# Kernel optimization log

Hardware: AMD Instinct MI355X
Metric: run time of the kernel (lower is better)

The kernel has to match this reference:

```python
import jax, jax.numpy as jnp
import numpy as np

B, T, S, E, H, V, OOV = 16, 32, 400, 128, 512, 32000, 50


def setup_inputs() -> dict:
    key = jax.random.key(0)
    ks = jax.random.split(key, 24)
    sc = 0.05
    inp = {
        'input_embeddings': jax.random.normal(ks[0], (B, T, E), jnp.float32),
        'h0': jax.random.normal(ks[1], (B, H), jnp.float32) * sc,
        'c0': jax.random.normal(ks[2], (B, H), jnp.float32) * sc,
        'encoder_outputs': jax.random.normal(ks[3], (B, S, H), jnp.float32),
        'encoder_masks': jnp.ones((B, S), jnp.float32),
        'extra_zeros': jnp.zeros((B, OOV), jnp.float32),
        'extended_source_idx': jax.random.randint(ks[4], (B, S), 0, V + OOV),
        # LSTM cell params (torch gate order i,f,g,o)
        'W_ih': jax.random.normal(ks[5], (4 * H, E), jnp.float32) * sc,
        'W_hh': jax.random.normal(ks[6], (4 * H, H), jnp.float32) * sc,
        'b_ih': jax.random.normal(ks[7], (4 * H,), jnp.float32) * sc,
        'b_hh': jax.random.normal(ks[8], (4 * H,), jnp.float32) * sc,
        # vocab projection
        'W_vocab': jax.random.normal(ks[9], (V, H), jnp.float32) * sc,
        'b_vocab': jax.random.normal(ks[10], (V,), jnp.float32) * sc,
        # attention: coverage_linear (H,1), energy_linear (H, 2H), v (H)
        'W_cov': jax.random.normal(ks[11], (H, 1), jnp.float32) * sc,
        'W_energy': jax.random.normal(ks[12], (H, 2 * H), jnp.float32) * sc,
        'b_energy': jax.random.normal(ks[13], (H,), jnp.float32) * sc,
        'v_attn': jax.random.uniform(ks[14], (H,), jnp.float32),
        # x_context: (E, E+H)
        'W_xctx': jax.random.normal(ks[15], (E, E + H), jnp.float32) * sc,
        'b_xctx': jax.random.normal(ks[16], (E,), jnp.float32) * sc,
        # attention_dense: (H, 2H)
        'W_ad': jax.random.normal(ks[17], (H, 2 * H), jnp.float32) * sc,
        'b_ad': jax.random.normal(ks[18], (H,), jnp.float32) * sc,
        # p_gen: (1, H + H + E)
        'W_pgen': jax.random.normal(ks[19], (1, 2 * H + E), jnp.float32) * sc,
        'b_pgen': jax.random.normal(ks[20], (1,), jnp.float32) * sc,
    }
    return inp


def _forward(input_embeddings, h0, c0, encoder_outputs, encoder_masks, extra_zeros,
             W_ih, W_hh, b_ih, b_hh, W_vocab, b_vocab, W_cov, W_energy, b_energy,
             v_attn, W_xctx, b_xctx, W_ad, b_ad, W_pgen, b_pgen, extended_source_idx):
    Bc, Sc_, Hc = encoder_outputs.shape
    oov = extra_zeros.shape[1]
    # split energy linear into decoder-part and encoder-part (cat order: [dec, enc])
    W_d, W_e = W_energy[:, :Hc], W_energy[:, Hc:]
    # encoder projection computed ONCE (same math as per-step recompute)
    enc_proj = jnp.einsum('bsh,kh->bsk', encoder_outputs, W_e) + b_energy  # [B,S,H]
    w_cov = W_cov[:, 0]  # [H]
    rows = jnp.arange(Bc)[:, None]

    def step(carry, emb_t):
        h, c, ctx, cov = carry  # [B,H],[B,H],[B,H],[B,S]
        x = jnp.concatenate([emb_t, ctx], -1) @ W_xctx.T + b_xctx  # [B,E]
        gates = x @ W_ih.T + b_ih + h @ W_hh.T + b_hh
        i_g, f_g, g_g, o_g = jnp.split(gates, 4, axis=-1)
        c = jax.nn.sigmoid(f_g) * c + jax.nn.sigmoid(i_g) * jnp.tanh(g_g)
        h = jax.nn.sigmoid(o_g) * jnp.tanh(c)
        # additive attention with coverage
        dec_proj = h @ W_d.T  # [B,H]
        cov_feat = cov[:, :, None] * w_cov[None, None, :]  # [B,S,H]
        energy = jnp.tanh(dec_proj[:, None, :] + enc_proj + cov_feat)
        score = jnp.einsum('bsh,h->bs', energy, v_attn)
        probs = jax.nn.softmax(score, axis=-1) * encoder_masks
        probs = probs / (probs.sum(-1, keepdims=True) + 1e-12)
        ctx = jnp.einsum('bs,bsh->bh', probs, encoder_outputs)
        cov = cov + probs
        # vocab distribution
        hh = jnp.concatenate([h, ctx], -1) @ W_ad.T + b_ad
        vocab_dist = jax.nn.softmax(hh @ W_vocab.T + b_vocab, axis=-1)  # [B,V]
        # pointer-generator mix
        p_gen = jax.nn.sigmoid(jnp.concatenate([ctx, h, x], -1) @ W_pgen.T + b_pgen)  # [B,1]
        attn_ = (1.0 - p_gen) * probs  # [B,S]
        ext = jnp.concatenate([vocab_dist * p_gen, extra_zeros], axis=1)  # [B,V+oov]
        final = ext.at[rows, extended_source_idx].add(attn_)
        return (h, c, ctx, cov), (final, probs, cov)

    init = (h0, c0, jnp.zeros_like(h0), jnp.zeros((Bc, Sc_), h0.dtype))
    (_, _, _, _), (finals, attns, covs) = jax.lax.scan(
        step, init, jnp.swapaxes(input_embeddings, 0, 1))
    return jnp.swapaxes(finals, 0, 1)  # [B,T,V+oov]


def reference(input_embeddings, h0, c0, encoder_outputs, encoder_masks, extra_zeros,
              extended_source_idx, W_ih, W_hh, b_ih, b_hh, W_vocab, b_vocab,
              W_cov, W_energy, b_energy, v_attn, W_xctx, b_xctx, W_ad, b_ad,
              W_pgen, b_pgen):
    return _forward(input_embeddings, h0, c0, encoder_outputs, encoder_masks,
                    extra_zeros, W_ih, W_hh, b_ih, b_hh, W_vocab, b_vocab,
                    W_cov, W_energy, b_energy, v_attn, W_xctx, b_xctx,
                    W_ad, b_ad, W_pgen, b_pgen, extended_source_idx)
```

## Files before the change

kernel.cpp:

```cpp
#include <hip/hip_runtime.h>
#include <hip/hip_bf16.h>
#include <cstddef>

namespace {

constexpr int B = 16, T = 32, S = 400, E = 128, H = 512, V = 32000, OOV = 50, VEXT = V + OOV;

typedef __attribute__((ext_vector_type(8))) short short8v;
typedef __attribute__((ext_vector_type(4))) float f32x4;

__device__ __forceinline__ float fsig(float x){ return 1.0f/(1.0f+__expf(-x)); }
__device__ __forceinline__ float ftanh(float x){
  float ax = fabsf(x);
  float t = __expf(-2.0f*ax);
  float r = (1.0f - t)/(1.0f + t);
  return copysignf(r, x);
}
__device__ __forceinline__ unsigned short f2bf(float f){
  unsigned int u = __float_as_uint(f);
  unsigned int r = (u + 0x7FFFu + ((u >> 16) & 1u)) >> 16;
  return (unsigned short)r;
}
__device__ __forceinline__ float bf2f(unsigned short u){
  return __uint_as_float(((unsigned)u) << 16);
}

__global__ __launch_bounds__(256) void k_init(const float* __restrict__ enc,
    const float* __restrict__ h0, const float* __restrict__ c0,
    unsigned short* __restrict__ enc_bf, float* __restrict__ harr,
    float* __restrict__ cbuf, float* __restrict__ cov, float* __restrict__ vsum){
  const int stride = gridDim.x*256;
  for (int i = blockIdx.x*256 + threadIdx.x; i < B*S*H; i += stride){
    enc_bf[i] = f2bf(enc[i]);
    if (i < B*H){ harr[i] = h0[i]; cbuf[i] = c0[i]; }
    if (i < B*S) cov[i] = 0.0f;
    if (i < T*B) vsum[i] = 0.0f;
  }
}

__global__ __launch_bounds__(128) void k_x0(const float* __restrict__ emb,
    const float* __restrict__ W_xctx, const float* __restrict__ b_xctx,
    float* __restrict__ x0){
  const int b = blockIdx.x, tid = threadIdx.x;
  __shared__ float se[E];
  se[tid] = emb[(size_t)(b*T)*E + tid];
  __syncthreads();
  const float* w = W_xctx + (size_t)tid*(E+H);
  float acc = b_xctx[tid];
  #pragma unroll 8
  for (int k=0;k<E;k+=4){
    float4 wv = *reinterpret_cast<const float4*>(w+k);
    acc += se[k]*wv.x + se[k+1]*wv.y + se[k+2]*wv.z + se[k+3]*wv.w;
  }
  x0[b*E + tid] = acc;
}

__global__ __launch_bounds__(256) void k_trw2(const float* __restrict__ W_energy,
    float* __restrict__ Wt, float* __restrict__ WdT){
  __shared__ float tile[32][33];
  const int z = blockIdx.z;
  float* out = z ? WdT : Wt;
  const int off = z ? 0 : H;
  const int j0 = blockIdx.x*32, k0 = blockIdx.y*32;
  const int tx = threadIdx.x & 31, ty = threadIdx.x >> 5;
  #pragma unroll
  for (int r=0;r<4;++r)
    tile[ty+8*r][tx] = W_energy[(size_t)(k0+ty+8*r)*(2*H) + off + j0 + tx];
  __syncthreads();
  #pragma unroll
  for (int r=0;r<4;++r)
    out[(size_t)(j0+ty+8*r)*H + k0 + tx] = tile[tx][ty+8*r];
}

__global__ __launch_bounds__(512) void k_encproj(const float* __restrict__ enc,
                          const float* __restrict__ Wt,
                          const float* __restrict__ b_energy,
                          unsigned short* __restrict__ enc_proj){
  const int r0 = blockIdx.x*16, k = threadIdx.x;
  const float* eb = enc + (size_t)r0*H;
  float acc[16];
  #pragma unroll
  for (int r=0;r<16;++r) acc[r]=0.0f;
  for (int j=0;j<H;j+=4){
    const float w0 = Wt[(size_t) j   *H + k];
    const float w1 = Wt[(size_t)(j+1)*H + k];
    const float w2 = Wt[(size_t)(j+2)*H + k];
    const float w3 = Wt[(size_t)(j+3)*H + k];
    #pragma unroll
    for (int r=0;r<16;++r){
      acc[r] += eb[(size_t)r*H + j]*w0 + eb[(size_t)r*H + j+1]*w1
              + eb[(size_t)r*H + j+2]*w2 + eb[(size_t)r*H + j+3]*w3;
    }
  }
  const float be = b_energy[k];
  #pragma unroll
  for (int r=0;r<16;++r) enc_proj[(size_t)(r0+r)*H + k] = f2bf(acc[r] + be);
}

__global__ __launch_bounds__(256) void k_gates2(
    const float* __restrict__ x, const float* __restrict__ hold,
    const float* __restrict__ W_ih, const float* __restrict__ W_hh,
    float* __restrict__ gpart){
  const int blk = blockIdx.x, tid = threadIdx.x;
  const int gbh = blk >> 2, kh = blk & 3;
  const int gb = gbh >> 1, bh = gbh & 1, b0 = bh*8;
  __shared__ float xh[8][640];
  __shared__ float sg[4][64][9];
  for (int b=0;b<8;++b)
    for (int k=tid;k<640;k+=256)
      xh[b][k] = (k<E) ? x[(b0+b)*E + k] : hold[(b0+b)*H + (k-E)];
  __syncthreads();
  const int w = tid >> 6, l = tid & 63, g = l >> 4, jj = l & 15;
  const int row = g*H + gb*16 + jj;
  float acc[8];
  #pragma unroll
  for (int b=0;b<8;++b) acc[b]=0.0f;
  const int ks = kh*160 + w*40, ke = ks + 40;
  const int k1 = (ke < 128) ? ke : 128;
  if (ks < 128){
    const float* wr = W_ih + (size_t)row*E;
    for (int k=ks; k<k1; k+=4){
      const float4 wv = *reinterpret_cast<const float4*>(wr + k);
      #pragma unroll
      for (int b=0;b<8;++b){
        const float4 xv = *reinterpret_cast<const float4*>(&xh[b][k]);
        acc[b] += xv.x*wv.x + xv.y*wv.y + xv.z*wv.z + xv.w*wv.w;
      }
    }
  }
  const int k2 = (ks > 128) ? ks : 128;
  if (k2 < ke){
    const float* wr = W_hh + (size_t)row*H - 128;
    for (int k=k2; k<ke; k+=4){
      const float4 wv = *reinterpret_cast<const float4*>(wr + k);
      #pragma unroll
      for (int b=0;b<8;++b){
        const float4 xv = *reinterpret_cast<const float4*>(&xh[b][k]);
        acc[b] += xv.x*wv.x + xv.y*wv.y + xv.z*wv.z + xv.w*wv.w;
      }
    }
  }
  #pragma unroll
  for (int b=0;b<8;++b) sg[w][l][b] = acc[b];
  __syncthreads();
  for (int i=tid; i<512; i+=256){
    const int l2 = i & 63, b = i >> 6;
    const int g2 = l2 >> 4, j2 = l2 & 15;
    const int row2 = g2*H + gb*16 + j2;
    gpart[((size_t)kh*B + (b0+b))*(4*H) + row2] =
        sg[0][l2][b]+sg[1][l2][b]+sg[2][l2][b]+sg[3][l2][b];
  }
}

__global__ __launch_bounds__(256) void k_dec2(const float* __restrict__ gpart,
    const float* __restrict__ cold, const float* __restrict__ b_ih,
    const float* __restrict__ b_hh, const float* __restrict__ WdT,
    float* __restrict__ cnew, float* __restrict__ hnew, float* __restrict__ dec){
  const int blk = blockIdx.x, tid = threadIdx.x;
  const int jc = blk >> 3, bp = blk & 7, b0 = bp*2;
  __shared__ float sh[2][H];
  __shared__ float r[4][64][2];
  for (int i=tid; i<2*H; i+=256){
    const int bl = i >> 9, j = i & 511;
    const int b = b0 + bl;
    float gs[4];
    #pragma unroll
    for (int g=0; g<4; ++g){
      const int row = g*H + j;
      float v = b_ih[row] + b_hh[row];
      #pragma unroll
      for (int kh=0; kh<4; ++kh) v += gpart[((size_t)kh*B + b)*(4*H) + row];
      gs[g] = v;
    }
    const float ig = fsig(gs[0]);
    const float fg = fsig(gs[1]);
    const float gg = ftanh(gs[2]);
    const float og = fsig(gs[3]);
    const float cn = fg*cold[b*H + j] + ig*gg;
    const float hn = og*ftanh(cn);
    cnew[b*H + j] = cn;
    hnew[b*H + j] = hn;
    sh[bl][j] = hn;
  }
  __syncthreads();
  const int w = tid >> 6, lane = tid & 63;
  const int j = jc*64 + lane;
  float a0=0.0f, a1=0.0f;
  for (int k=w*128; k<w*128+128; ++k){
    const float wv = WdT[(size_t)k*H + j];
    a0 += sh[0][k]*wv;
    a1 += sh[1][k]*wv;
  }
  r[w][lane][0]=a0; r[w][lane][1]=a1;
  __syncthreads();
  if (tid < 128){
    const int jl = tid & 63, bb = tid >> 6;
    dec[(b0+bb)*H + jc*64 + jl] = r[0][jl][bb]+r[1][jl][bb]+r[2][jl][bb]+r[3][jl][bb];
  }
}

__global__ __launch_bounds__(256) void k_score(const float* __restrict__ dec_proj,
    const unsigned short* __restrict__ encp, const float* __restrict__ W_cov,
    const float* __restrict__ v_attn, const float* __restrict__ cov,
    float* __restrict__ score, float* __restrict__ xnext){
  const int b = blockIdx.y;
  if (blockIdx.x==0 && threadIdx.x < E) xnext[b*E + threadIdx.x] = 0.0f;
  const int wave = threadIdx.x >> 6, lane = threadIdx.x & 63;
  const int s = blockIdx.x*4 + wave;
  const float cv = cov[b*S + s];
  const int k0 = lane*8;
  const short8v ev = *reinterpret_cast<const short8v*>(encp + (size_t)(b*S + s)*H + k0);
  const float* dp = dec_proj + b*H;
  float acc = 0.0f;
  #pragma unroll
  for (int u=0;u<8;++u){
    const int k = k0+u;
    acc += ftanh(dp[k] + bf2f((unsigned short)ev[u]) + cv*W_cov[k]) * v_attn[k];
  }
  #pragma unroll
  for (int off=32; off>0; off>>=1) acc += __shfl_down(acc, off);
  if (lane==0) score[b*S + s] = acc;
}

__global__ __launch_bounds__(256) void k_ctx(const float* __restrict__ score,
    const float* __restrict__ masks, const unsigned short* __restrict__ enc_bf,
    const float* __restrict__ emb, int tnext,
    const float* __restrict__ W_xctx, const float* __restrict__ b_xctx,
    float* __restrict__ cov, float* __restrict__ probs_t,
    float* __restrict__ ctx_t, float* __restrict__ xnext){
  const int b = blockIdx.x, hc = blockIdx.y, tid = threadIdx.x;
  __shared__ float red[256], sp[512], sctx[64], se[E];
  if (tid < E) se[tid] = emb[(size_t)(b*T + tnext)*E + tid];
  const float sc0 = (tid < S)      ? score[b*S + tid]       : -1e30f;
  const float sc1 = (tid+256 < S)  ? score[b*S + tid + 256] : -1e30f;
  red[tid] = fmaxf(sc0, sc1);
  __syncthreads();
  for (int off=128; off>0; off>>=1){ if (tid<off) red[tid]=fmaxf(red[tid],red[tid+off]); __syncthreads(); }
  const float mx = red[0];
  __syncthreads();
  const float e0 = (tid < S)     ? __expf(sc0 - mx) : 0.0f;
  const float e1 = (tid+256 < S) ? __expf(sc1 - mx) : 0.0f;
  red[tid] = e0 + e1;
  __syncthreads();
  for (int off=128; off>0; off>>=1){ if (tid<off) red[tid]+=red[tid+off]; __syncthreads(); }
  const float den = red[0];
  __syncthreads();
  const float p0 = (tid < S)     ? (e0/den)*masks[b*S+tid]     : 0.0f;
  const float p1 = (tid+256 < S) ? (e1/den)*masks[b*S+tid+256] : 0.0f;
  red[tid] = p0 + p1;
  __syncthreads();
  for (int off=128; off>0; off>>=1){ if (tid<off) red[tid]+=red[tid+off]; __syncthreads(); }
  const float inv = 1.0f/(red[0] + 1e-12f);
  __syncthreads();
  const float pr0 = p0*inv, pr1 = p1*inv;
  sp[tid] = pr0; sp[tid+256] = pr1;
  if (hc==0){
    if (tid < S){ probs_t[b*S+tid] = pr0; cov[b*S+tid] += pr0; }
    if (tid+256 < S){ probs_t[b*S+tid+256] = pr1; cov[b*S+tid+256] += pr1; }
  }
  __syncthreads();
  {
    const int c = tid & 63, sg_ = tid >> 6;
    const unsigned short* eb = enc_bf + (size_t)b*S*H + hc*64 + c;
    float a = 0.0f;
    for (int s=sg_; s<S; s+=4) a += sp[s]*bf2f(eb[(size_t)s*H]);
    red[tid] = a;
    __syncthreads();
    if (tid < 64){
      const float cval = red[tid]+red[tid+64]+red[tid+128]+red[tid+192];
      sctx[tid] = cval;
      ctx_t[b*H + hc*64 + tid] = cval;
    }
  }
  __syncthreads();
  if (tid < E){
    const float* wr = W_xctx + (size_t)tid*(E+H);
    float acc = 0.0f;
    #pragma unroll
    for (int k=0;k<64;k+=4){
      const float4 wc = *reinterpret_cast<const float4*>(wr + E + hc*64 + k);
      acc += sctx[k]*wc.x + sctx[k+1]*wc.y + sctx[k+2]*wc.z + sctx[k+3]*wc.w;
    }
    #pragma unroll
    for (int k=0;k<16;k+=4){
      const float4 we = *reinterpret_cast<const float4*>(wr + hc*16 + k);
      const float* eb2 = se + hc*16 + k;
      acc += eb2[0]*we.x + eb2[1]*we.y + eb2[2]*we.z + eb2[3]*we.w;
    }
    if (hc==0) acc += b_xctx[tid];
    atomicAdd(&xnext[b*E + tid], acc);
  }
}

__global__ __launch_bounds__(512) void k_hhgemm(const float* __restrict__ harr,
    const float* __restrict__ ctx_all, const float* __restrict__ W_ad,
    const float* __restrict__ b_ad, float* __restrict__ hh_all){
  __shared__ unsigned short ldsA[256][72];
  __shared__ unsigned short ldsB[128][72];
  const int tid = threadIdx.x, lane = tid & 63, w = tid >> 6;
  const int wm = w >> 1, wn = w & 1;
  const int m0 = (int)blockIdx.y * 256;
  const int n0 = (int)blockIdx.x * 128;
  const int nl = lane & 15, kg = lane >> 4;
  f32x4 acc[4][4];
  #pragma unroll
  for (int mf=0;mf<4;++mf)
    #pragma unroll
    for (int nf=0;nf<4;++nf) acc[mf][nf] = (f32x4){0.f,0.f,0.f,0.f};
  for (int kc=0; kc<16; ++kc){
    __syncthreads();
    for (int j = tid; j < 4096; j += 512){
      const int row = j >> 4, c4 = j & 15;
      const int kk_ = kc*64 + c4*4;
      const float* src = (kk_ < H)
        ? (harr + (size_t)(m0+row+B)*H + kk_)
        : (ctx_all + (size_t)(m0+row)*H + (kk_ - H));
      const float4 v = *reinterpret_cast<const float4*>(src);
      ushort4 u; u.x=f2bf(v.x); u.y=f2bf(v.y); u.z=f2bf(v.z); u.w=f2bf(v.w);
      *reinterpret_cast<ushort4*>(&ldsA[row][c4*4]) = u;
    }
    for (int j = tid; j < 2048; j += 512){
      const int row = j >> 4, c4 = j & 15;
      const float4 v = *reinterpret_cast<const float4*>(
          W_ad + (size_t)(n0+row)*(2*H) + kc*64 + c4*4);
      ushort4 u; u.x=f2bf(v.x); u.y=f2bf(v.y); u.z=f2bf(v.z); u.w=f2bf(v.w);
      *reinterpret_cast<ushort4*>(&ldsB[row][c4*4]) = u;
    }
    __syncthreads();
    #pragma unroll
    for (int kk=0; kk<2; ++kk){
      short8v a[4], bf[4];
      #pragma unroll
      for (int mf=0;mf<4;++mf)
        a[mf] = *reinterpret_cast<const short8v*>(&ldsA[wm*64 + mf*16 + nl][kk*32 + kg*8]);
      #pragma unroll
      for (int nf=0;nf<4;++nf)
        bf[nf] = *reinterpret_cast<const short8v*>(&ldsB[wn*64 + nf*16 + nl][kk*32 + kg*8]);
      #pragma unroll
      for (int mf=0;mf<4;++mf)
        #pragma unroll
        for (int nf=0;nf<4;++nf)
          acc[mf][nf] = __builtin_amdgcn_mfma_f32_16x16x32_bf16(a[mf], bf[nf], acc[mf][nf], 0, 0, 0);
    }
  }
  #pragma unroll
  for (int mf=0;mf<4;++mf){
    #pragma unroll
    for (int r=0;r<4;++r){
      const int m = m0 + wm*64 + mf*16 + kg*4 + r;
      #pragma unroll
      for (int nf=0;nf<4;++nf){
        const int n = n0 + wn*64 + nf*16 + nl;
        hh_all[(size_t)m*H + n] = acc[mf][nf][r] + b_ad[n];
      }
    }
  }
}

__global__ __launch_bounds__(256) void k_pgen(const float* __restrict__ ctx_all,
    const float* __restrict__ harr, const float* __restrict__ x_all,
    const float* __restrict__ W_pgen, const float* __restrict__ b_pgen,
    float* __restrict__ praw){
  const int m = blockIdx.x*4 + (threadIdx.x >> 6);
  const int lane = threadIdx.x & 63;
  float part = 0.0f;
  for (int k = lane; k < 2*H+E; k += 64){
    float v;
    if (k < H)        v = ctx_all[(size_t)m*H + k];
    else if (k < 2*H) v = harr[(size_t)(m+B)*H + (k-H)];
    else              v = x_all[(size_t)m*E + (k-2*H)];
    part += v * W_pgen[k];
  }
  #pragma unroll
  for (int off=32; off>0; off>>=1) part += __shfl_down(part, off);
  if (lane==0) praw[m] = part + b_pgen[0];
}

__global__ __launch_bounds__(512) void k_vocab3(
    const float* __restrict__ hh_all,
    const float* __restrict__ W_vocab, const float* __restrict__ b_vocab,
    float* __restrict__ out, float* __restrict__ vsum){
  __shared__ unsigned short ldsA[256][72];
  __shared__ unsigned short ldsB[128][72];
  __shared__ float svs[256];
  const int tid = threadIdx.x, lane = tid & 63, w = tid >> 6;
  const int wm = w >> 1, wn = w & 1;
  const int m0 = (int)blockIdx.y * 256;
  const int n0 = (int)blockIdx.x * 128;
  const int nl = lane & 15, kg = lane >> 4;
  if (tid < 256) svs[tid] = 0.0f;
  f32x4 acc[4][4];
  #pragma unroll
  for (int mf=0;mf<4;++mf)
    #pragma unroll
    for (int nf=0;nf<4;++nf) acc[mf][nf] = (f32x4){0.f,0.f,0.f,0.f};
  for (int kc=0; kc<8; ++kc){
    __syncthreads();
    for (int j = tid; j < 4096; j += 512){
      const int row = j >> 4, c4 = j & 15;
      const float4 v = *reinterpret_cast<const float4*>(
          hh_all + (size_t)(m0+row)*H + kc*64 + c4*4);
      ushort4 u; u.x=f2bf(v.x); u.y=f2bf(v.y); u.z=f2bf(v.z); u.w=f2bf(v.w);
      *reinterpret_cast<ushort4*>(&ldsA[row][c4*4]) = u;
    }
    for (int j = tid; j < 2048; j += 512){
      const int row = j >> 4, c4 = j & 15;
      const float4 v = *reinterpret_cast<const float4*>(
          W_vocab + (size_t)(n0+row)*H + kc*64 + c4*4);
      ushort4 u; u.x=f2bf(v.x); u.y=f2bf(v.y); u.z=f2bf(v.z); u.w=f2bf(v.w);
      *reinterpret_cast<ushort4*>(&ldsB[row][c4*4]) = u;
    }
    __syncthreads();
    #pragma unroll
    for (int kk=0; kk<2; ++kk){
      short8v a[4], bf[4];
      #pragma unroll
      for (int mf=0;mf<4;++mf)
        a[mf] = *reinterpret_cast<const short8v*>(&ldsA[wm*64 + mf*16 + nl][kk*32 + kg*8]);
      #pragma unroll
      for (int nf=0;nf<4;++nf)
        bf[nf] = *reinterpret_cast<const short8v*>(&ldsB[wn*64 + nf*16 + nl][kk*32 + kg*8]);
      #pragma unroll
      for (int mf=0;mf<4;++mf)
        #pragma unroll
        for (int nf=0;nf<4;++nf)
          acc[mf][nf] = __builtin_amdgcn_mfma_f32_16x16x32_bf16(a[mf], bf[nf], acc[mf][nf], 0, 0, 0);
    }
  }
  float bv[4];
  #pragma unroll
  for (int nf=0;nf<4;++nf) bv[nf] = b_vocab[n0 + wn*64 + nf*16 + nl];
  #pragma unroll
  for (int mf=0;mf<4;++mf){
    #pragma unroll
    for (int r=0;r<4;++r){
      const int m = m0 + wm*64 + mf*16 + kg*4 + r;
      const int tq = m >> 4, bq = m & 15;
      float* orow = out + ((size_t)bq*T + tq)*VEXT;
      float s = 0.0f;
      #pragma unroll
      for (int nf=0;nf<4;++nf){
        const int n = n0 + wn*64 + nf*16 + nl;
        const float e = __expf(acc[mf][nf][r] + bv[nf]);
        orow[n] = e;
        s += e;
      }
      s += __shfl_xor(s, 1);
      s += __shfl_xor(s, 2);
      s += __shfl_xor(s, 4);
      s += __shfl_xor(s, 8);
      if (nl == 0) atomicAdd(&svs[m - m0], s);
    }
  }
  __syncthreads();
  for (int i = tid; i < 256; i += 512) atomicAdd(&vsum[m0 + i], svs[i]);
}

__global__ __launch_bounds__(256) void k_finalize(const float* __restrict__ praw,
    const float* __restrict__ vsum, const float* __restrict__ exz,
    float* __restrict__ out){
  const int rm = blockIdx.x, vc = blockIdx.y, tid = threadIdx.x;
  const int t = rm >> 4, b = rm & 15;
  float* orow = out + ((size_t)b*T + t)*VEXT;
  if (vc < 8){
    const float scl = fsig(praw[rm]) / vsum[rm];
    const int base = vc*4000;
    for (int i = tid; i < 4000; i += 256) orow[base + i] *= scl;
  } else if (tid < OOV){
    orow[V + tid] = exz[b*OOV + tid];
  }
}

__global__ __launch_bounds__(256) void k_scatter_all(const float* __restrict__ probs_all,
    const float* __restrict__ praw, const int* __restrict__ eidx,
    float* __restrict__ out){
  const int stride = gridDim.x*256;
  for (int i = blockIdx.x*256 + threadIdx.x; i < T*B*S; i += stride){
    const int t = i / (B*S);
    const int rem = i - t*B*S;
    const int b = rem / S, s = rem - b*S;
    const float fac = 1.0f - fsig(praw[t*B + b]);
    float* orow = out + ((size_t)b*T + t)*VEXT;
    atomicAdd(&orow[eidx[b*S + s]], fac*probs_all[(size_t)(t*B + b)*S + s]);
  }
}

}

extern "C" void kernel_launch(void* const* d_in, const int* in_sizes, int n_in,
                              void* d_out, int out_size, void* d_ws, size_t ws_size,
                              hipStream_t stream){
  const float* emb    = (const float*)d_in[0];
  const float* h0     = (const float*)d_in[1];
  const float* c0     = (const float*)d_in[2];
  const float* enc    = (const float*)d_in[3];
  const float* masks  = (const float*)d_in[4];
  const float* exz    = (const float*)d_in[5];
  const int*   eidx   = (const int*)d_in[6];
  const float* W_ih   = (const float*)d_in[7];
  const float* W_hh   = (const float*)d_in[8];
  const float* b_ih   = (const float*)d_in[9];
  const float* b_hh   = (const float*)d_in[10];
  const float* W_vocab= (const float*)d_in[11];
  const float* b_vocab= (const float*)d_in[12];
  const float* W_cov  = (const float*)d_in[13];
  const float* W_energy=(const float*)d_in[14];
  const float* b_energy=(const float*)d_in[15];
  const float* v_attn = (const float*)d_in[16];
  const float* W_xctx = (const float*)d_in[17];
  const float* b_xctx = (const float*)d_in[18];
  const float* W_ad   = (const float*)d_in[19];
  const float* b_ad   = (const float*)d_in[20];
  const float* W_pgen = (const float*)d_in[21];
  const float* b_pgen = (const float*)d_in[22];

  float* ws = (float*)d_ws;
  float* cbuf     = ws;
  float* x_all    = ws + 16384;
  float* dec      = ws + 83968;
  float* score    = ws + 92160;
  float* cov      = ws + 98560;
  float* praw     = ws + 104960;
  float* vsum     = ws + 105472;
  float* probs_all= ws + 105984;
  float* harr     = ws + 310784;
  float* ctx_all  = ws + 581120;
  float* hh_all   = ws + 843264;
  float* WdT      = ws + 1105408;
  float* Wt       = ws + 1367552;
  float* gpart    = ws + 1629696;
  unsigned short* enc_bf = (unsigned short*)(ws + 1760768);
  unsigned short* encp   = (unsigned short*)(ws + 3399168);
  float* outp     = (float*)d_out;

  k_init<<<300,256,0,stream>>>(enc,h0,c0,enc_bf,harr,cbuf,cov,vsum);
  k_x0<<<16,128,0,stream>>>(emb,W_xctx,b_xctx,x_all);
  k_trw2<<<dim3(16,16,2),256,0,stream>>>(W_energy,Wt,WdT);
  k_encproj<<<400,512,0,stream>>>(enc,Wt,b_energy,encp);

  for (int t=0;t<T;++t){
    const int p = t&1;
    const float* cold = cbuf + p*8192;
    float* cnew = cbuf + (p^1)*8192;
    const int tnext = (t+1 < T) ? (t+1) : (T-1);
    k_gates2<<<256,256,0,stream>>>(x_all + (size_t)t*B*E, harr + (size_t)t*B*H,
                                   W_ih, W_hh, gpart);
    k_dec2<<<64,256,0,stream>>>(gpart, cold, b_ih, b_hh, WdT,
                                cnew, harr + (size_t)(t+1)*B*H, dec);
    k_score<<<dim3(100,16),256,0,stream>>>(dec, encp, W_cov, v_attn, cov, score,
                                           x_all + (size_t)(t+1)*B*E);
    k_ctx<<<dim3(16,8),256,0,stream>>>(score, masks, enc_bf, emb, tnext,
        W_xctx, b_xctx, cov, probs_all + (size_t)t*B*S,
        ctx_all + (size_t)t*B*H, x_all + (size_t)(t+1)*B*E);
  }

  k_hhgemm<<<dim3(4,2),512,0,stream>>>(harr, ctx_all, W_ad, b_ad, hh_all);
  k_pgen<<<128,256,0,stream>>>(ctx_all, harr, x_all, W_pgen, b_pgen, praw);
  k_vocab3<<<dim3(250,2),512,0,stream>>>(hh_all, W_vocab, b_vocab, outp, vsum);
  k_finalize<<<dim3(512,9),256,0,stream>>>(praw, vsum, exz, outp);
  k_scatter_all<<<200,256,0,stream>>>(probs_all, praw, eidx, outp);
}
```

Baseline: 2.084 ms.

## Fuse LSTM cell, decoder projection and attention scoring; retile hh GEMM

Merges the LSTM cell update, decoder-state projection and attention score computation into one kernel per step. Each of 64 blocks (16 batches × 4 source chunks) recomputes the cell and the full 512x512 projection for its batch row, which removes one launch per step and the dec round-trip through global memory. The cost is 4x redundant projection work and far fewer blocks than before (64 vs 64+1600). Separately, the post-loop hh GEMM uses smaller 128x64 tiles so it launches 32 blocks instead of 8, trading per-block reuse for more parallelism.

```diff
diff --git a/kernel.cpp b/kernel.cpp
--- a/kernel.cpp
+++ b/kernel.cpp
@@ -152,17 +152,19 @@
   }
 }
 
-__global__ __launch_bounds__(256) void k_dec2(const float* __restrict__ gpart,
-    const float* __restrict__ cold, const float* __restrict__ b_ih,
-    const float* __restrict__ b_hh, const float* __restrict__ WdT,
-    float* __restrict__ cnew, float* __restrict__ hnew, float* __restrict__ dec){
-  const int blk = blockIdx.x, tid = threadIdx.x;
-  const int jc = blk >> 3, bp = blk & 7, b0 = bp*2;
-  __shared__ float sh[2][H];
-  __shared__ float r[4][64][2];
-  for (int i=tid; i<2*H; i+=256){
-    const int bl = i >> 9, j = i & 511;
-    const int b = b0 + bl;
+__global__ __launch_bounds__(256) void k_decscore(
+    const float* __restrict__ gpart, const float* __restrict__ cold,
+    const float* __restrict__ b_ih, const float* __restrict__ b_hh,
+    const float* __restrict__ WdT, const unsigned short* __restrict__ encp,
+    const float* __restrict__ W_cov, const float* __restrict__ v_attn,
+    const float* __restrict__ cov,
+    float* __restrict__ cnew, float* __restrict__ hnew,
+    float* __restrict__ score, float* __restrict__ xnext){
+  const int b = blockIdx.x, sc = blockIdx.y, tid = threadIdx.x;
+  __shared__ float sh[H], sdec[H], swc[H], sva[H];
+  #pragma unroll
+  for (int jj=0; jj<2; ++jj){
+    const int j = tid + jj*256;
     float gs[4];
     #pragma unroll
     for (int g=0; g<4; ++g){
@@ -178,48 +180,45 @@
     const float og = fsig(gs[3]);
     const float cn = fg*cold[b*H + j] + ig*gg;
     const float hn = og*ftanh(cn);
-    cnew[b*H + j] = cn;
-    hnew[b*H + j] = hn;
-    sh[bl][j] = hn;
-  }
-  __syncthreads();
-  const int w = tid >> 6, lane = tid & 63;
-  const int j = jc*64 + lane;
-  float a0=0.0f, a1=0.0f;
-  for (int k=w*128; k<w*128+128; ++k){
-    const float wv = WdT[(size_t)k*H + j];
-    a0 += sh[0][k]*wv;
-    a1 += sh[1][k]*wv;
-  }
-  r[w][lane][0]=a0; r[w][lane][1]=a1;
-  __syncthreads();
-  if (tid < 128){
-    const int jl = tid & 63, bb = tid >> 6;
-    dec[(b0+bb)*H + jc*64 + jl] = r[0][jl][bb]+r[1][jl][bb]+r[2][jl][bb]+r[3][jl][bb];
-  }
-}
-
-__global__ __launch_bounds__(256) void k_score(const float* __restrict__ dec_proj,
-    const unsigned short* __restrict__ encp, const float* __restrict__ W_cov,
-    const float* __restrict__ v_attn, const float* __restrict__ cov,
-    float* __restrict__ score, float* __restrict__ xnext){
-  const int b = blockIdx.y;
-  if (blockIdx.x==0 && threadIdx.x < E) xnext[b*E + threadIdx.x] = 0.0f;
-  const int wave = threadIdx.x >> 6, lane = threadIdx.x & 63;
-  const int s = blockIdx.x*4 + wave;
-  const float cv = cov[b*S + s];
-  const int k0 = lane*8;
-  const short8v ev = *reinterpret_cast<const short8v*>(encp + (size_t)(b*S + s)*H + k0);
-  const float* dp = dec_proj + b*H;
-  float acc = 0.0f;
-  #pragma unroll
-  for (int u=0;u<8;++u){
-    const int k = k0+u;
-    acc += ftanh(dp[k] + bf2f((unsigned short)ev[u]) + cv*W_cov[k]) * v_attn[k];
-  }
-  #pragma unroll
-  for (int off=32; off>0; off>>=1) acc += __shfl_down(acc, off);
-  if (lane==0) score[b*S + s] = acc;
+    if (sc==0){ cnew[b*H + j] = cn; hnew[b*H + j] = hn; }
+    sh[j] = hn;
+    swc[j] = W_cov[j];
+    sva[j] = v_attn[j];
+  }
+  if (sc==0 && tid < E) xnext[b*E + tid] = 0.0f;
+  __syncthreads();
+  {
+    float a0 = 0.0f, a1 = 0.0f;
+    const int j0 = tid, j1 = tid + 256;
+    #pragma unroll 4
+    for (int k=0; k<H; ++k){
+      const float hv = sh[k];
+      const float* wr = WdT + (size_t)k*H;
+      a0 += hv*wr[j0];
+      a1 += hv*wr[j1];
+    }
+    sdec[j0] = a0;
+    sdec[j1] = a1;
+  }
+  __syncthreads();
+  {
+    const int wid = tid >> 6, lane = tid & 63, k0 = lane*8;
+    const int s0 = sc*100;
+    for (int s = s0 + wid; s < s0 + 100; s += 4){
+      const float cv = cov[b*S + s];
+      const short8v ev = *reinterpret_cast<const short8v*>(
+          encp + (size_t)(b*S + s)*H + k0);
+      float a = 0.0f;
+      #pragma unroll
+      for (int u=0;u<8;++u){
+        const int k = k0+u;
+        a += ftanh(sdec[k] + bf2f((unsigned short)ev[u]) + cv*swc[k]) * sva[k];
+      }
+      #pragma unroll
+      for (int off=32; off>0; off>>=1) a += __shfl_down(a, off);
+      if (lane==0) score[b*S + s] = a;
+    }
+  }
 }
 
 __global__ __launch_bounds__(256) void k_ctx(const float* __restrict__ score,
@@ -295,21 +294,19 @@
 __global__ __launch_bounds__(512) void k_hhgemm(const float* __restrict__ harr,
     const float* __restrict__ ctx_all, const float* __restrict__ W_ad,
     const float* __restrict__ b_ad, float* __restrict__ hh_all){
-  __shared__ unsigned short ldsA[256][72];
-  __shared__ unsigned short ldsB[128][72];
+  __shared__ unsigned short ldsA[128][72];
+  __shared__ unsigned short ldsB[64][72];
   const int tid = threadIdx.x, lane = tid & 63, w = tid >> 6;
-  const int wm = w >> 1, wn = w & 1;
-  const int m0 = (int)blockIdx.y * 256;
-  const int n0 = (int)blockIdx.x * 128;
+  const int wm = w >> 2, wn = w & 3;
+  const int m0 = (int)blockIdx.y * 128;
+  const int n0 = (int)blockIdx.x * 64;
   const int nl = lane & 15, kg = lane >> 4;
-  f32x4 acc[4][4];
-  #pragma unroll
-  for (int mf=0;mf<4;++mf)
-    #pragma unroll
-    for (int nf=0;nf<4;++nf) acc[mf][nf] = (f32x4){0.f,0.f,0.f,0.f};
+  f32x4 acc[4];
+  #pragma unroll
+  for (int mf=0;mf<4;++mf) acc[mf] = (f32x4){0.f,0.f,0.f,0.f};
   for (int kc=0; kc<16; ++kc){
     __syncthreads();
-    for (int j = tid; j < 4096; j += 512){
+    for (int j = tid; j < 2048; j += 512){
       const int row = j >> 4, c4 = j & 15;
       const int kk_ = kc*64 + c4*4;
       const float* src = (kk_ < H)
@@ -319,7 +316,7 @@
       ushort4 u; u.x=f2bf(v.x); u.y=f2bf(v.y); u.z=f2bf(v.z); u.w=f2bf(v.w);
       *reinterpret_cast<ushort4*>(&ldsA[row][c4*4]) = u;
     }
-    for (int j = tid; j < 2048; j += 512){
+    for (int j = tid; j < 1024; j += 512){
       const int row = j >> 4, c4 = j & 15;
       const float4 v = *reinterpret_cast<const float4*>(
           W_ad + (size_t)(n0+row)*(2*H) + kc*64 + c4*4);
@@ -329,30 +326,22 @@
     __syncthreads();
     #pragma unroll
     for (int kk=0; kk<2; ++kk){
-      short8v a[4], bf[4];
-      #pragma unroll
-      for (int mf=0;mf<4;++mf)
-        a[mf] = *reinterpret_cast<const short8v*>(&ldsA[wm*64 + mf*16 + nl][kk*32 + kg*8]);
-      #pragma unroll
-      for (int nf=0;nf<4;++nf)
-        bf[nf] = *reinterpret_cast<const short8v*>(&ldsB[wn*64 + nf*16 + nl][kk*32 + kg*8]);
-      #pragma unroll
-      for (int mf=0;mf<4;++mf)
-        #pragma unroll
-        for (int nf=0;nf<4;++nf)
-          acc[mf][nf] = __builtin_amdgcn_mfma_f32_16x16x32_bf16(a[mf], bf[nf], acc[mf][nf], 0, 0, 0);
-    }
-  }
+      const short8v bfr = *reinterpret_cast<const short8v*>(&ldsB[wn*16 + nl][kk*32 + kg*8]);
+      #pragma unroll
+      for (int mf=0;mf<4;++mf){
+        const short8v a = *reinterpret_cast<const short8v*>(&ldsA[wm*64 + mf*16 + nl][kk*32 + kg*8]);
+        acc[mf] = __builtin_amdgcn_mfma_f32_16x16x32_bf16(a, bfr, acc[mf], 0, 0, 0);
+      }
+    }
+  }
+  const int n = n0 + wn*16 + nl;
+  const float bv = b_ad[n];
   #pragma unroll
   for (int mf=0;mf<4;++mf){
     #pragma unroll
     for (int r=0;r<4;++r){
       const int m = m0 + wm*64 + mf*16 + kg*4 + r;
-      #pragma unroll
-      for (int nf=0;nf<4;++nf){
-        const int n = n0 + wn*64 + nf*16 + nl;
-        hh_all[(size_t)m*H + n] = acc[mf][nf][r] + b_ad[n];
-      }
+      hh_all[(size_t)m*H + n] = acc[mf][r] + bv;
     }
   }
 }
@@ -517,20 +506,19 @@
   float* ws = (float*)d_ws;
   float* cbuf     = ws;
   float* x_all    = ws + 16384;
-  float* dec      = ws + 83968;
-  float* score    = ws + 92160;
-  float* cov      = ws + 98560;
-  float* praw     = ws + 104960;
-  float* vsum     = ws + 105472;
-  float* probs_all= ws + 105984;
-  float* harr     = ws + 310784;
-  float* ctx_all  = ws + 581120;
-  float* hh_all   = ws + 843264;
-  float* WdT      = ws + 1105408;
-  float* Wt       = ws + 1367552;
-  float* gpart    = ws + 1629696;
-  unsigned short* enc_bf = (unsigned short*)(ws + 1760768);
-  unsigned short* encp   = (unsigned short*)(ws + 3399168);
+  float* score    = ws + 83968;
+  float* cov      = ws + 90368;
+  float* praw     = ws + 96768;
+  float* vsum     = ws + 97280;
+  float* probs_all= ws + 97792;
+  float* harr     = ws + 302592;
+  float* ctx_all  = ws + 572928;
+  float* hh_all   = ws + 835072;
+  float* WdT      = ws + 1097216;
+  float* Wt       = ws + 1359360;
+  float* gpart    = ws + 1621504;
+  unsigned short* enc_bf = (unsigned short*)(ws + 1752576);
+  unsigned short* encp   = (unsigned short*)(ws + 3390976);
   float* outp     = (float*)d_out;
 
   k_init<<<300,256,0,stream>>>(enc,h0,c0,enc_bf,harr,cbuf,cov,vsum);
@@ -545,16 +533,15 @@
     const int tnext = (t+1 < T) ? (t+1) : (T-1);
     k_gates2<<<256,256,0,stream>>>(x_all + (size_t)t*B*E, harr + (size_t)t*B*H,
                                    W_ih, W_hh, gpart);
-    k_dec2<<<64,256,0,stream>>>(gpart, cold, b_ih, b_hh, WdT,
-                                cnew, harr + (size_t)(t+1)*B*H, dec);
-    k_score<<<dim3(100,16),256,0,stream>>>(dec, encp, W_cov, v_attn, cov, score,
-                                           x_all + (size_t)(t+1)*B*E);
+    k_decscore<<<dim3(16,4),256,0,stream>>>(gpart, cold, b_ih, b_hh, WdT, encp,
+        W_cov, v_attn, cov, cnew, harr + (size_t)(t+1)*B*H, score,
+        x_all + (size_t)(t+1)*B*E);
     k_ctx<<<dim3(16,8),256,0,stream>>>(score, masks, enc_bf, emb, tnext,
         W_xctx, b_xctx, cov, probs_all + (size_t)t*B*S,
         ctx_all + (size_t)t*B*H, x_all + (size_t)(t+1)*B*E);
   }
 
-  k_hhgemm<<<dim3(4,2),512,0,stream>>>(harr, ctx_all, W_ad, b_ad, hh_all);
+  k_hhgemm<<<dim3(8,4),512,0,stream>>>(harr, ctx_all, W_ad, b_ad, hh_all);
   k_pgen<<<128,256,0,stream>>>(ctx_all, harr, x_all, W_pgen, b_pgen, praw);
   k_vocab3<<<dim3(250,2),512,0,stream>>>(hh_all, W_vocab, b_vocab, outp, vsum);
   k_finalize<<<dim3(512,9),256,0,stream>>>(praw, vsum, exz, outp);
```

Result: slower. 3.444 ms (+65.3%).

## Use bf16 MFMA GEMM for encoder projection and retile hh GEMM

Applied to the files above, without the earlier changes.

Replaces the scalar FP32 encoder-projection kernel with a bf16 MFMA tiled GEMM (256x128 tiles) that reads W_energy directly, which also removes the separate transpose into Wt. Separately, the post-loop hh GEMM moves to smaller 128x64 tiles with 32 blocks instead of 8, so more compute units are in use. The projection inputs are now rounded to bf16 before the multiply, a small precision change, and the smaller hh tiles reuse less data per block.

```diff
diff --git a/kernel.cpp b/kernel.cpp
--- a/kernel.cpp
+++ b/kernel.cpp
@@ -55,46 +55,83 @@
   x0[b*E + tid] = acc;
 }
 
-__global__ __launch_bounds__(256) void k_trw2(const float* __restrict__ W_energy,
-    float* __restrict__ Wt, float* __restrict__ WdT){
+__global__ __launch_bounds__(256) void k_trw(const float* __restrict__ W_energy,
+                                             float* __restrict__ WdT){
   __shared__ float tile[32][33];
-  const int z = blockIdx.z;
-  float* out = z ? WdT : Wt;
-  const int off = z ? 0 : H;
   const int j0 = blockIdx.x*32, k0 = blockIdx.y*32;
   const int tx = threadIdx.x & 31, ty = threadIdx.x >> 5;
   #pragma unroll
   for (int r=0;r<4;++r)
-    tile[ty+8*r][tx] = W_energy[(size_t)(k0+ty+8*r)*(2*H) + off + j0 + tx];
+    tile[ty+8*r][tx] = W_energy[(size_t)(k0+ty+8*r)*(2*H) + j0 + tx];
   __syncthreads();
   #pragma unroll
   for (int r=0;r<4;++r)
-    out[(size_t)(j0+ty+8*r)*H + k0 + tx] = tile[tx][ty+8*r];
-}
-
-__global__ __launch_bounds__(512) void k_encproj(const float* __restrict__ enc,
-                          const float* __restrict__ Wt,
-                          const float* __restrict__ b_energy,
-                          unsigned short* __restrict__ enc_proj){
-  const int r0 = blockIdx.x*16, k = threadIdx.x;
-  const float* eb = enc + (size_t)r0*H;
-  float acc[16];
-  #pragma unroll
-  for (int r=0;r<16;++r) acc[r]=0.0f;
-  for (int j=0;j<H;j+=4){
-    const float w0 = Wt[(size_t) j   *H + k];
-    const float w1 = Wt[(size_t)(j+1)*H + k];
-    const float w2 = Wt[(size_t)(j+2)*H + k];
-    const float w3 = Wt[(size_t)(j+3)*H + k];
-    #pragma unroll
-    for (int r=0;r<16;++r){
-      acc[r] += eb[(size_t)r*H + j]*w0 + eb[(size_t)r*H + j+1]*w1
-              + eb[(size_t)r*H + j+2]*w2 + eb[(size_t)r*H + j+3]*w3;
-    }
-  }
-  const float be = b_energy[k];
-  #pragma unroll
-  for (int r=0;r<16;++r) enc_proj[(size_t)(r0+r)*H + k] = f2bf(acc[r] + be);
+    WdT[(size_t)(j0+ty+8*r)*H + k0 + tx] = tile[tx][ty+8*r];
+}
+
+__global__ __launch_bounds__(512) void k_encproj2(const float* __restrict__ enc,
+    const float* __restrict__ W_energy, const float* __restrict__ b_energy,
+    unsigned short* __restrict__ enc_proj){
+  __shared__ unsigned short ldsA[256][72];
+  __shared__ unsigned short ldsB[128][72];
+  const int tid = threadIdx.x, lane = tid & 63, w = tid >> 6;
+  const int wm = w >> 1, wn = w & 1;
+  const int m0 = (int)blockIdx.y * 256;
+  const int n0 = (int)blockIdx.x * 128;
+  const int nl = lane & 15, kg = lane >> 4;
+  f32x4 acc[4][4];
+  #pragma unroll
+  for (int mf=0;mf<4;++mf)
+    #pragma unroll
+    for (int nf=0;nf<4;++nf) acc[mf][nf] = (f32x4){0.f,0.f,0.f,0.f};
+  for (int kc=0; kc<8; ++kc){
+    __syncthreads();
+    for (int j = tid; j < 4096; j += 512){
+      const int row = j >> 4, c4 = j & 15;
+      const float4 v = *reinterpret_cast<const float4*>(
+          enc + (size_t)(m0+row)*H + kc*64 + c4*4);
+      ushort4 u; u.x=f2bf(v.x); u.y=f2bf(v.y); u.z=f2bf(v.z); u.w=f2bf(v.w);
+      *reinterpret_cast<ushort4*>(&ldsA[row][c4*4]) = u;
+    }
+    for (int j = tid; j < 2048; j += 512){
+      const int row = j >> 4, c4 = j & 15;
+      const float4 v = *reinterpret_cast<const float4*>(
+          W_energy + (size_t)(n0+row)*(2*H) + H + kc*64 + c4*4);
+      ushort4 u; u.x=f2bf(v.x); u.y=f2bf(v.y); u.z=f2bf(v.z); u.w=f2bf(v.w);
+      *reinterpret_cast<ushort4*>(&ldsB[row][c4*4]) = u;
+    }
+    __syncthreads();
+    #pragma unroll
+    for (int kk=0; kk<2; ++kk){
+      short8v a[4], bf[4];
+      #pragma unroll
+      for (int mf=0;mf<4;++mf)
+        a[mf] = *reinterpret_cast<const short8v*>(&ldsA[wm*64 + mf*16 + nl][kk*32 + kg*8]);
+      #pragma unroll
+      for (int nf=0;nf<4;++nf)
+        bf[nf] = *reinterpret_cast<const short8v*>(&ldsB[wn*64 + nf*16 + nl][kk*32 + kg*8]);
+      #pragma unroll
+      for (int mf=0;mf<4;++mf)
+        #pragma unroll
+        for (int nf=0;nf<4;++nf)
+          acc[mf][nf] = __builtin_amdgcn_mfma_f32_16x16x32_bf16(a[mf], bf[nf], acc[mf][nf], 0, 0, 0);
+    }
+  }
+  float bv[4];
+  #pragma unroll
+  for (int nf=0;nf<4;++nf) bv[nf] = b_energy[n0 + wn*64 + nf*16 + nl];
+  #pragma unroll
+  for (int mf=0;mf<4;++mf){
+    #pragma unroll
+    for (int r=0;r<4;++r){
+      const int m = m0 + wm*64 + mf*16 + kg*4 + r;
+      #pragma unroll
+      for (int nf=0;nf<4;++nf){
+        const int n = n0 + wn*64 + nf*16 + nl;
+        enc_proj[(size_t)m*H + n] = f2bf(acc[mf][nf][r] + bv[nf]);
+      }
+    }
+  }
 }
 
 __global__ __launch_bounds__(256) void k_gates2(
@@ -295,21 +332,19 @@
 __global__ __launch_bounds__(512) void k_hhgemm(const float* __restrict__ harr,
     const float* __restrict__ ctx_all, const float* __restrict__ W_ad,
     const float* __restrict__ b_ad, float* __restrict__ hh_all){
-  __shared__ unsigned short ldsA[256][72];
-  __shared__ unsigned short ldsB[128][72];
+  __shared__ unsigned short ldsA[128][72];
+  __shared__ unsigned short ldsB[64][72];
   const int tid = threadIdx.x, lane = tid & 63, w = tid >> 6;
-  const int wm = w >> 1, wn = w & 1;
-  const int m0 = (int)blockIdx.y * 256;
-  const int n0 = (int)blockIdx.x * 128;
+  const int wm = w >> 2, wn = w & 3;
+  const int m0 = (int)blockIdx.y * 128;
+  const int n0 = (int)blockIdx.x * 64;
   const int nl = lane & 15, kg = lane >> 4;
-  f32x4 acc[4][4];
-  #pragma unroll
-  for (int mf=0;mf<4;++mf)
-    #pragma unroll
-    for (int nf=0;nf<4;++nf) acc[mf][nf] = (f32x4){0.f,0.f,0.f,0.f};
+  f32x4 acc[4];
+  #pragma unroll
+  for (int mf=0;mf<4;++mf) acc[mf] = (f32x4){0.f,0.f,0.f,0.f};
   for (int kc=0; kc<16; ++kc){
     __syncthreads();
-    for (int j = tid; j < 4096; j += 512){
+    for (int j = tid; j < 2048; j += 512){
       const int row = j >> 4, c4 = j & 15;
       const int kk_ = kc*64 + c4*4;
       const float* src = (kk_ < H)
@@ -319,7 +354,7 @@
       ushort4 u; u.x=f2bf(v.x); u.y=f2bf(v.y); u.z=f2bf(v.z); u.w=f2bf(v.w);
       *reinterpret_cast<ushort4*>(&ldsA[row][c4*4]) = u;
     }
-    for (int j = tid; j < 2048; j += 512){
+    for (int j = tid; j < 1024; j += 512){
       const int row = j >> 4, c4 = j & 15;
       const float4 v = *reinterpret_cast<const float4*>(
           W_ad + (size_t)(n0+row)*(2*H) + kc*64 + c4*4);
@@ -329,30 +364,22 @@
     __syncthreads();
     #pragma unroll
     for (int kk=0; kk<2; ++kk){
-      short8v a[4], bf[4];
-      #pragma unroll
-      for (int mf=0;mf<4;++mf)
-        a[mf] = *reinterpret_cast<const short8v*>(&ldsA[wm*64 + mf*16 + nl][kk*32 + kg*8]);
-      #pragma unroll
-      for (int nf=0;nf<4;++nf)
-        bf[nf] = *reinterpret_cast<const short8v*>(&ldsB[wn*64 + nf*16 + nl][kk*32 + kg*8]);
-      #pragma unroll
-      for (int mf=0;mf<4;++mf)
-        #pragma unroll
-        for (int nf=0;nf<4;++nf)
-          acc[mf][nf] = __builtin_amdgcn_mfma_f32_16x16x32_bf16(a[mf], bf[nf], acc[mf][nf], 0, 0, 0);
-    }
-  }
+      const short8v bfr = *reinterpret_cast<const short8v*>(&ldsB[wn*16 + nl][kk*32 + kg*8]);
+      #pragma unroll
+      for (int mf=0;mf<4;++mf){
+        const short8v a = *reinterpret_cast<const short8v*>(&ldsA[wm*64 + mf*16 + nl][kk*32 + kg*8]);
+        acc[mf] = __builtin_amdgcn_mfma_f32_16x16x32_bf16(a, bfr, acc[mf], 0, 0, 0);
+      }
+    }
+  }
+  const int n = n0 + wn*16 + nl;
+  const float bv = b_ad[n];
   #pragma unroll
   for (int mf=0;mf<4;++mf){
     #pragma unroll
     for (int r=0;r<4;++r){
       const int m = m0 + wm*64 + mf*16 + kg*4 + r;
-      #pragma unroll
-      for (int nf=0;nf<4;++nf){
-        const int n = n0 + wn*64 + nf*16 + nl;
-        hh_all[(size_t)m*H + n] = acc[mf][nf][r] + b_ad[n];
-      }
+      hh_all[(size_t)m*H + n] = acc[mf][r] + bv;
     }
   }
 }
@@ -527,16 +554,15 @@
   float* ctx_all  = ws + 581120;
   float* hh_all   = ws + 843264;
   float* WdT      = ws + 1105408;
-  float* Wt       = ws + 1367552;
-  float* gpart    = ws + 1629696;
-  unsigned short* enc_bf = (unsigned short*)(ws + 1760768);
-  unsigned short* encp   = (unsigned short*)(ws + 3399168);
+  float* gpart    = ws + 1367552;
+  unsigned short* enc_bf = (unsigned short*)(ws + 1498624);
+  unsigned short* encp   = (unsigned short*)(ws + 3137024);
   float* outp     = (float*)d_out;
 
   k_init<<<300,256,0,stream>>>(enc,h0,c0,enc_bf,harr,cbuf,cov,vsum);
   k_x0<<<16,128,0,stream>>>(emb,W_xctx,b_xctx,x_all);
-  k_trw2<<<dim3(16,16,2),256,0,stream>>>(W_energy,Wt,WdT);
-  k_encproj<<<400,512,0,stream>>>(enc,Wt,b_energy,encp);
+  k_trw<<<dim3(16,16),256,0,stream>>>(W_energy,WdT);
+  k_encproj2<<<dim3(4,25),512,0,stream>>>(enc,W_energy,b_energy,encp);
 
   for (int t=0;t<T;++t){
     const int p = t&1;
@@ -554,7 +580,7 @@
         ctx_all + (size_t)t*B*H, x_all + (size_t)(t+1)*B*E);
   }
 
-  k_hhgemm<<<dim3(4,2),512,0,stream>>>(harr, ctx_all, W_ad, b_ad, hh_all);
+  k_hhgemm<<<dim3(8,4),512,0,stream>>>(harr, ctx_all, W_ad, b_ad, hh_all);
   k_pgen<<<128,256,0,stream>>>(ctx_all, harr, x_all, W_pgen, b_pgen, praw);
   k_vocab3<<<dim3(250,2),512,0,stream>>>(hh_all, W_vocab, b_vocab, outp, vsum);
   k_finalize<<<dim3(512,9),256,0,stream>>>(praw, vsum, exz, outp);
```

Result: faster. 2.002 ms, median of 2 (-4.0%).
